# Kernel tuning notes

Hardware: AMD Instinct MI355X
Metric: run time of the kernel (lower is better)

Reference implementation:

```python
import jax, jax.numpy as jnp
import numpy as np
import math

CUTOFF = 5.0
F = 128
N_ATOMS = 4096
N_EDGES = 16384

# ---------- Clebsch-Gordan coefficients in the real spherical-harmonic basis ----------

def _cgc(l1, l2, l3, m1, m2, m3):
    if m1 + m2 != m3 or l3 < abs(l1 - l2) or l3 > l1 + l2:
        return 0.0
    f = math.factorial
    pre = math.sqrt((2 * l3 + 1) * f(l3 + l1 - l2) * f(l3 - l1 + l2) * f(l1 + l2 - l3) / f(l1 + l2 + l3 + 1))
    pre *= math.sqrt(f(l3 + m3) * f(l3 - m3) * f(l1 - m1) * f(l1 + m1) * f(l2 - m2) * f(l2 + m2))
    s = 0.0
    for k in range(l1 + l2 - l3 + 1):
        a = [k, l1 + l2 - l3 - k, l1 - m1 - k, l2 + m2 - k, l3 - l2 + m1 + k, l3 - l1 - m2 + k]
        if min(a) < 0:
            continue
        d = 1.0
        for t in a:
            d *= f(t)
        s += (-1) ** k / d
    return pre * s

def _umat(l):
    # complex SH in terms of real SH (rows: complex m, cols: real m, offset by l)
    U = np.zeros((2 * l + 1, 2 * l + 1), dtype=np.complex128)
    U[l, l] = 1.0
    for m in range(1, l + 1):
        U[l + m, l + m] = (-1) ** m / math.sqrt(2)
        U[l + m, l - m] = 1j * (-1) ** m / math.sqrt(2)
        U[l - m, l + m] = 1.0 / math.sqrt(2)
        U[l - m, l - m] = -1j / math.sqrt(2)
    return U

def _real_cg(l1, l2, l3):
    cg = np.zeros((2 * l1 + 1, 2 * l2 + 1, 2 * l3 + 1), dtype=np.complex128)
    for i, m1 in enumerate(range(-l1, l1 + 1)):
        for j, m2 in enumerate(range(-l2, l2 + 1)):
            m3 = m1 + m2
            if abs(m3) <= l3:
                cg[i, j, l3 + m3] = _cgc(l1, l2, l3, m1, m2, m3)
    U1, U2, U3 = _umat(l1), _umat(l2), _umat(l3)
    C = np.einsum('abc,aA,bB,cC->ABC', cg, U1, U2, np.conj(U3))
    return np.real(C).astype(np.float32)

# coupling paths (l1 from bond basis 0..2, l2 from atom features 0..4, output l3 0..4);
# even l1+l2+l3 keeps proper tensors only (include_pseudotensors=False)
PATHS = [(l1, l2, l3) for l1 in range(3) for l2 in range(5) for l3 in range(5)
         if abs(l1 - l2) <= l3 <= l1 + l2 and (l1 + l2 + l3) % 2 == 0]
CG_TABLES = [_real_cg(*p) for p in PATHS]

# ---------- equivariant building blocks ----------

def _seg(l):
    return slice(l * l, (l + 1) * (l + 1))

def edense(x, W, b):
    # per-degree channel mixing; bias only on the scalar (l=0) channel
    L = W.shape[0] - 1
    outs = []
    for l in range(L + 1):
        o = jnp.einsum('epmf,fg->epmg', x[:, :, _seg(l), :], W[l])
        if l == 0:
            o = o + b
        outs.append(o)
    return jnp.concatenate(outs, axis=-2)

def normalize(x, eps=1e-6):
    n2 = jnp.sum(x * x, axis=-2, keepdims=True)
    return x * jax.lax.rsqrt(n2 + eps)

def gated_mish(x):
    s = x[..., 0:1, :]
    sp = jax.nn.softplus(s)
    t = jnp.tanh(sp)
    ms = s * t
    dm = t + s * (1.0 - t * t) * jax.nn.sigmoid(s)
    return jnp.concatenate([ms, x[..., 1:, :] * dm], axis=-2)

def real_sph_harm(u):
    # Racah-normalized real SH up to l=2, m ordered -l..l (cartesian_order=False)
    x, y, z = u[:, 0], u[:, 1], u[:, 2]
    s3 = math.sqrt(3.0)
    return jnp.stack([
        jnp.ones_like(x),
        y, z, x,
        s3 * x * y, s3 * y * z, 0.5 * (3.0 * z * z - 1.0), s3 * x * z, 0.5 * s3 * (x * x - y * y),
    ], axis=-1)  # (E, 9)

def basis_expansion(disp):
    r = jnp.sqrt(jnp.sum(disp * disp, axis=-1) + 1e-12)  # (E,)
    sh = real_sph_harm(disp / r[:, None])                 # (E, 9)
    k = jnp.arange(F, dtype=disp.dtype)
    rad = jnp.cos(k[None, :] * (jnp.pi * r[:, None] / CUTOFF))  # basic_fourier, (E, F)
    uc = r / CUTOFF
    denom = jnp.maximum(1.0 - uc * uc, 1e-9)
    cut = jnp.where(uc < 1.0, jnp.exp(1.0 - 1.0 / denom), 0.0)  # smooth_cutoff
    rad = rad * cut[:, None]
    return sh[:, None, :, None] * rad[:, None, None, :]  # (E, 1, 9, F)

def tensor_product(x1, x2, w_tp):
    # CG tensor product (FusedTensor math): per-path learnable per-feature weights
    E, Ff = x1.shape[0], x1.shape[-1]
    out = jnp.zeros((E, 1, 25, Ff), dtype=x1.dtype)
    for p, (l1, l2, l3) in enumerate(PATHS):
        C = jnp.asarray(CG_TABLES[p])
        a = x1[:, 0, _seg(l1), :]
        b = x2[:, 0, _seg(l2), :]
        seg = jnp.einsum('abc,eaf,ebf->ecf', C, a, b)
        out = out.at[:, 0, _seg(l3), :].add(seg * w_tp[p][None, None, :])
    return out

# ---------- harness ----------

def setup_inputs() -> dict:
    key = jax.random.key(0)
    ks = jax.random.split(key, 8)
    sc = 1.0 / math.sqrt(F)
    return {
        'atomic_descriptors': jax.random.normal(ks[0], (N_ATOMS, 1, 25, F), jnp.float32),
        'neighbour_indices': jax.random.randint(ks[1], (N_EDGES, 2), 0, N_ATOMS),
        'neighbour_displacements': jax.random.normal(ks[2], (N_EDGES, 3), jnp.float32),
        'W1': jax.random.normal(ks[3], (5, F, F), jnp.float32) * sc,
        'b1': jnp.zeros((F,), jnp.float32),
        'W2': jax.random.normal(ks[4], (5, F, F), jnp.float32) * sc,
        'b2': jnp.zeros((F,), jnp.float32),
        'W3': jax.random.normal(ks[5], (3, F, F), jnp.float32) * sc,
        'b3': jnp.zeros((F,), jnp.float32),
        'w_tp': jax.random.normal(ks[6], (len(PATHS), F), jnp.float32),
    }

def reference(atomic_descriptors, neighbour_indices, neighbour_displacements, W1, b1, W2, b2, W3, b3, w_tp):
    i, j = neighbour_indices[:, 0], neighbour_indices[:, 1]
    y = atomic_descriptors[i] + atomic_descriptors[j]       # (E, 1, 25, F)
    y = edense(y, W1, b1)
    y = normalize(y)
    y = gated_mish(y)
    y = edense(y, W2, b2) + y
    be = basis_expansion(neighbour_displacements)           # (E, 1, 9, F)
    bd = edense(be, W3, b3)
    return tensor_product(bd, y, w_tp)                      # (E, 1, 25, F)
```

## Files before the change

### kernel.cpp

```cpp
#include <hip/hip_runtime.h>
#include <math.h>

#ifndef M_PI
#define M_PI 3.14159265358979323846
#endif

namespace {

constexpr int NF = 128;
constexpr int NM = 25;

struct CD { double re, im; };
constexpr CD cmulc(CD x, CD y){ return CD{x.re*y.re - x.im*y.im, x.re*y.im + x.im*y.re}; }

constexpr double cfact(int n){ double r = 1.0; for (int i = 2; i <= n; ++i) r *= (double)i; return r; }

constexpr double csqrt_(double x){
  if (x <= 0.0) return 0.0;
  double g = x < 1.0 ? 1.0 : x;
  for (int i = 0; i < 48; ++i) g = 0.5 * (g + x / g);
  return g;
}

constexpr double cgc_(int l1, int l2, int l3, int m1, int m2, int m3){
  if (m1 + m2 != m3) return 0.0;
  int dmin = l1 > l2 ? l1 - l2 : l2 - l1;
  if (l3 < dmin || l3 > l1 + l2) return 0.0;
  double pre = csqrt_((2.0*l3 + 1.0) * cfact(l3 + l1 - l2) * cfact(l3 - l1 + l2) *
                      cfact(l1 + l2 - l3) / cfact(l1 + l2 + l3 + 1));
  pre *= csqrt_(cfact(l3 + m3) * cfact(l3 - m3) * cfact(l1 - m1) * cfact(l1 + m1) *
                cfact(l2 - m2) * cfact(l2 + m2));
  double s = 0.0;
  for (int k = 0; k <= l1 + l2 - l3; ++k){
    int a0 = k, a1 = l1 + l2 - l3 - k, a2 = l1 - m1 - k;
    int a3 = l2 + m2 - k, a4 = l3 - l2 + m1 + k, a5 = l3 - l1 - m2 + k;
    if (a0 < 0 || a1 < 0 || a2 < 0 || a3 < 0 || a4 < 0 || a5 < 0) continue;
    double d = cfact(a0)*cfact(a1)*cfact(a2)*cfact(a3)*cfact(a4)*cfact(a5);
    s += ((k & 1) ? -1.0 : 1.0) / d;
  }
  return pre * s;
}

constexpr CD umat(int l, int a, int A){
  const double is2 = 0.70710678118654752440;
  int ma = a - l, mA = A - l;
  if (ma == 0) return (mA == 0) ? CD{1.0, 0.0} : CD{0.0, 0.0};
  if (ma > 0){
    double sg = (ma & 1) ? -1.0 : 1.0;
    if (mA ==  ma) return CD{sg * is2, 0.0};
    if (mA == -ma) return CD{0.0, sg * is2};
    return CD{0.0, 0.0};
  }
  if (mA == -ma) return CD{is2, 0.0};
  if (mA ==  ma) return CD{0.0, -is2};
  return CD{0.0, 0.0};
}

struct TpEntry { int a, b, c, p; float v; };
struct TpTable { TpEntry e[1024]; int n; int npaths; };

constexpr TpTable build_tp(){
  TpTable T{};
  T.n = 0;
  int p = 0;
  for (int l1 = 0; l1 < 3; ++l1)
  for (int l2 = 0; l2 < 5; ++l2)
  for (int l3 = 0; l3 < 5; ++l3){
    int dmin = l1 > l2 ? l1 - l2 : l2 - l1;
    if (l3 < dmin || l3 > l1 + l2) continue;
    if ((l1 + l2 + l3) & 1) continue;
    double Cr[5][9][9] = {};
    for (int a = 0; a <= 2*l1; ++a)
    for (int b = 0; b <= 2*l2; ++b){
      int m1 = a - l1, m2 = b - l2, m3 = m1 + m2;
      if (m3 < -l3 || m3 > l3) continue;
      double cg = cgc_(l1, l2, l3, m1, m2, m3);
      if (cg == 0.0) continue;
      int c3 = l3 + m3;
      int Al[2] = { l1 + m1, l1 - m1 }; int nA = (m1 == 0) ? 1 : 2;
      int Bl[2] = { l2 + m2, l2 - m2 }; int nB = (m2 == 0) ? 1 : 2;
      int Cl[2] = { l3 + m3, l3 - m3 }; int nC = (m3 == 0) ? 1 : 2;
      for (int ia = 0; ia < nA; ++ia)
      for (int ib = 0; ib < nB; ++ib)
      for (int ic = 0; ic < nC; ++ic){
        CD u1 = umat(l1, a, Al[ia]);
        CD u2 = umat(l2, b, Bl[ib]);
        CD u3 = umat(l3, c3, Cl[ic]);
        CD t12 = cmulc(u1, u2);
        double re = t12.re * u3.re + t12.im * u3.im;
        Cr[Al[ia]][Bl[ib]][Cl[ic]] += cg * re;
      }
    }
    for (int A = 0; A <= 2*l1; ++A)
    for (int B = 0; B <= 2*l2; ++B)
    for (int Cc = 0; Cc <= 2*l3; ++Cc){
      double v = Cr[A][B][Cc];
      if (v > 1e-12 || v < -1e-12){
        T.e[T.n].a = l1*l1 + A;
        T.e[T.n].b = l2*l2 + B;
        T.e[T.n].c = l3*l3 + Cc;
        T.e[T.n].p = p;
        T.e[T.n].v = (float)v;
        ++T.n;
      }
    }
    ++p;
  }
  T.npaths = p;
  return T;
}

constexpr TpTable TPT = build_tp();
constexpr int TPN      = TPT.n;
constexpr int NPATHS_C = TPT.npaths;
static_assert(NPATHS_C == 23, "path count mismatch vs reference PATHS");
static_assert(TPN <= 1024, "TP table overflow");

struct TpSorted { TpEntry e[1024]; int n; int split; };
constexpr TpSorted sort_tp(){
  TpSorted S{}; S.n = TPT.n; S.split = 0;
  int k = 0;
  for (int half = 0; half < 2; ++half){
    for (int b = 0; b < NM; ++b)
      for (int t = 0; t < TPT.n; ++t){
        int h = (TPT.e[t].c >= 13) ? 1 : 0;
        if (h == half && TPT.e[t].b == b) S.e[k++] = TPT.e[t];
      }
    if (half == 0) S.split = k;
  }
  return S;
}
constexpr TpSorted STP = sort_tp();
static_assert(STP.n == TPN, "sort lost entries");
constexpr int TP_SPLIT = STP.split;

using bfrag = __attribute__((ext_vector_type(8))) short;
using f32x4 = __attribute__((ext_vector_type(4))) float;

__device__ __forceinline__ unsigned short bf16rn(float x){
  unsigned u = __float_as_uint(x);
  unsigned r = (u + 0x7FFFu + ((u >> 16) & 1u)) >> 16;
  return (unsigned short)r;
}
__device__ __forceinline__ float bfhi_to_f(unsigned short h){
  return __uint_as_float((unsigned)h << 16);
}

constexpr int T_STRIDE = 136;
constexpr int Y_STRIDE = 129;

__global__ __launch_bounds__(256) void prep_kernel(const float* __restrict__ W1,
                                                   const float* __restrict__ W2,
                                                   const float* __restrict__ W3,
                                                   short* __restrict__ W1hi, short* __restrict__ W1lo,
                                                   short* __restrict__ W2hi, short* __restrict__ W2lo,
                                                   short* __restrict__ W3hi, short* __restrict__ W3lo){
  const int t = blockIdx.x * 256 + threadIdx.x;
  if (t >= 26624) return;
  int arr, s;
  if (t < 10240)      { arr = 0; s = t; }
  else if (t < 20480) { arr = 1; s = t - 10240; }
  else                { arr = 2; s = t - 20480; }
  const int lane = s & 63;
  const int ks   = (s >> 6) & 3;
  const int nt   = (s >> 8) & 7;
  const int l    = s >> 11;
  const float* W = (arr == 0) ? W1 : (arr == 1) ? W2 : W3;
  short* Hi = (arr == 0) ? W1hi : (arr == 1) ? W2hi : W3hi;
  short* Lo = (arr == 0) ? W1lo : (arr == 1) ? W2lo : W3lo;
  const int g = 16 * nt + (lane & 15);
  short hi8[8], lo8[8];
  #pragma unroll
  for (int j = 0; j < 8; ++j){
    const int f = 32 * ks + 8 * (lane >> 4) + j;
    const float w = W[(l * NF + f) * NF + g];
    unsigned short h = bf16rn(w);
    hi8[j] = (short)h;
    lo8[j] = (short)bf16rn(w - bfhi_to_f(h));
  }
  const size_t off = (size_t)s * 8;
  *(bfrag*)(Hi + off) = *(bfrag*)hi8;
  *(bfrag*)(Lo + off) = *(bfrag*)lo8;
}

__device__ __forceinline__ void mfma_gemm(const unsigned short* tHi, const unsigned short* tLo,
                                          const short* __restrict__ Whi, const short* __restrict__ Wlo,
                                          int lane, int wave, f32x4 acc[5][2]){
  const int quad = lane >> 4, l16 = lane & 15;
  #pragma unroll
  for (int l = 0; l < 5; ++l){
    const int mb = l * l;
    #pragma unroll
    for (int ks = 0; ks < 4; ++ks){
      const bfrag ah = *(const bfrag*)&tHi[(mb + l16) * T_STRIDE + 32 * ks + 8 * quad];
      const bfrag al = *(const bfrag*)&tLo[(mb + l16) * T_STRIDE + 32 * ks + 8 * quad];
      #pragma unroll
      for (int n2 = 0; n2 < 2; ++n2){
        const int nt = 2 * wave + n2;
        const size_t off = ((size_t)((l * 8 + nt) * 4 + ks)) * 512 + lane * 8;
        const bfrag bh = *(const bfrag*)(Whi + off);
        const bfrag bl = *(const bfrag*)(Wlo + off);
        acc[l][n2] = __builtin_amdgcn_mfma_f32_16x16x32_bf16(ah, bh, acc[l][n2], 0, 0, 0);
        acc[l][n2] = __builtin_amdgcn_mfma_f32_16x16x32_bf16(al, bh, acc[l][n2], 0, 0, 0);
        acc[l][n2] = __builtin_amdgcn_mfma_f32_16x16x32_bf16(ah, bl, acc[l][n2], 0, 0, 0);
      }
    }
  }
}

__global__ __launch_bounds__(256, 4) void atoms_kernel(const float* __restrict__ A,
                                                       const short* __restrict__ W1hi,
                                                       const short* __restrict__ W1lo,
                                                       float* __restrict__ Z){
  __shared__ unsigned short aHi[32 * T_STRIDE];
  __shared__ unsigned short aLo[32 * T_STRIDE];
  const int n   = blockIdx.x;
  const int tid = threadIdx.x;
  const int f   = tid & 127, half = tid >> 7;
  const float* Ab = A + (size_t)n * NM * NF;

  const int m0 = half ? 13 : 0, m1 = half ? 25 : 13;
  for (int m = m0; m < m1; ++m){
    const float x = Ab[m * NF + f];
    const unsigned short h = bf16rn(x);
    aHi[m * T_STRIDE + f] = h;
    aLo[m * T_STRIDE + f] = bf16rn(x - bfhi_to_f(h));
  }
  if (half){
    for (int m = 25; m < 32; ++m){ aHi[m * T_STRIDE + f] = 0; aLo[m * T_STRIDE + f] = 0; }
  }
  __syncthreads();

  const int lane = tid & 63, wave = tid >> 6;
  f32x4 acc[5][2];
  #pragma unroll
  for (int l = 0; l < 5; ++l)
    #pragma unroll
    for (int n2 = 0; n2 < 2; ++n2)
      acc[l][n2] = f32x4{0.f, 0.f, 0.f, 0.f};

  mfma_gemm(aHi, aLo, W1hi, W1lo, lane, wave, acc);

  const int quad = lane >> 4, l16 = lane & 15;
  float* Zb = Z + (size_t)n * NM * NF;
  #pragma unroll
  for (int l = 0; l < 5; ++l)
    #pragma unroll
    for (int n2 = 0; n2 < 2; ++n2){
      const int col = 16 * (2 * wave + n2) + l16;
      #pragma unroll
      for (int r = 0; r < 4; ++r){
        if (r <= 2 * l){
          const int row = 4 * quad + r;
          if (row <= 2 * l)
            Zb[(l * l + row) * NF + col] = acc[l][n2][r];
        }
      }
    }
}

__global__ __launch_bounds__(256) void radial_kernel(const float* __restrict__ disp,
                                                     const short* __restrict__ W3hi,
                                                     const short* __restrict__ W3lo,
                                                     const float* __restrict__ b3,
                                                     float* __restrict__ out,
                                                     int n_edges){
  __shared__ unsigned short rHi[32 * T_STRIDE];
  __shared__ unsigned short rLo[32 * T_STRIDE];
  __shared__ float rbuf[32];
  __shared__ float cbuf[32];
  const int e0  = blockIdx.x * 32;
  const int tid = threadIdx.x;
  if (tid < 32){
    const int e = e0 + tid;
    float r = 1.f, cut = 0.f;
    if (e < n_edges){
      const float dx = disp[3 * e], dy = disp[3 * e + 1], dz = disp[3 * e + 2];
      r = sqrtf(dx * dx + dy * dy + dz * dz + 1e-12f);
      const float uc  = r * 0.2f;
      const float den = fmaxf(1.f - uc * uc, 1e-9f);
      cut = (uc < 1.f) ? expf(1.f - 1.f / den) : 0.f;
    }
    rbuf[tid] = r; cbuf[tid] = cut;
  }
  __syncthreads();

  const int f = tid & 127, half = tid >> 7;
  #pragma unroll
  for (int mr = 0; mr < 16; ++mr){
    const int m = half * 16 + mr;
    const float rad = cosf((float)f * ((float)M_PI * 0.2f) * rbuf[m]) * cbuf[m];
    const unsigned short h = bf16rn(rad);
    rHi[m * T_STRIDE + f] = h;
    rLo[m * T_STRIDE + f] = bf16rn(rad - bfhi_to_f(h));
  }
  __syncthreads();

  const int lane = tid & 63, wave = tid >> 6, quad = lane >> 4, l16 = lane & 15;
  f32x4 acc[2][3][2];
  #pragma unroll
  for (int mt = 0; mt < 2; ++mt)
    #pragma unroll
    for (int l = 0; l < 3; ++l)
      #pragma unroll
      for (int n2 = 0; n2 < 2; ++n2)
        acc[mt][l][n2] = f32x4{0.f, 0.f, 0.f, 0.f};

  #pragma unroll
  for (int mt = 0; mt < 2; ++mt){
    #pragma unroll
    for (int ks = 0; ks < 4; ++ks){
      const bfrag ah = *(const bfrag*)&rHi[(mt * 16 + l16) * T_STRIDE + 32 * ks + 8 * quad];
      const bfrag al = *(const bfrag*)&rLo[(mt * 16 + l16) * T_STRIDE + 32 * ks + 8 * quad];
      #pragma unroll
      for (int l = 0; l < 3; ++l){
        #pragma unroll
        for (int n2 = 0; n2 < 2; ++n2){
          const int nt = 2 * wave + n2;
          const size_t off = ((size_t)((l * 8 + nt) * 4 + ks)) * 512 + lane * 8;
          const bfrag bh = *(const bfrag*)(W3hi + off);
          const bfrag bl = *(const bfrag*)(W3lo + off);
          acc[mt][l][n2] = __builtin_amdgcn_mfma_f32_16x16x32_bf16(ah, bh, acc[mt][l][n2], 0, 0, 0);
          acc[mt][l][n2] = __builtin_amdgcn_mfma_f32_16x16x32_bf16(al, bh, acc[mt][l][n2], 0, 0, 0);
          acc[mt][l][n2] = __builtin_amdgcn_mfma_f32_16x16x32_bf16(ah, bl, acc[mt][l][n2], 0, 0, 0);
        }
      }
    }
  }

  #pragma unroll
  for (int mt = 0; mt < 2; ++mt)
    #pragma unroll
    for (int l = 0; l < 3; ++l)
      #pragma unroll
      for (int n2 = 0; n2 < 2; ++n2){
        const int col = 16 * (2 * wave + n2) + l16;
        #pragma unroll
        for (int rr = 0; rr < 4; ++rr){
          const int e = e0 + mt * 16 + 4 * quad + rr;
          if (e < n_edges){
            float v = acc[mt][l][n2][rr];
            if (l == 0) v += b3[col];
            out[(size_t)e * (NM * NF) + l * NF + col] = v;
          }
        }
      }
}

template<int CG>
__device__ __forceinline__ void tp_accum(const float* y2col ,
                                         const float bd[9], const float wp[NPATHS_C],
                                         float o[13]){
  constexpr int t0 = (CG == 0) ? 0 : TP_SPLIT;
  constexpr int t1 = (CG == 0) ? TP_SPLIT : TPN;
  constexpr int cbase = (CG == 0) ? 0 : 13;
  float y2b = 0.f;
  #pragma unroll
  for (int t = t0; t < t1; ++t){
    if (t == t0 || STP.e[t].b != STP.e[t-1].b)
      y2b = y2col[STP.e[t].b * Y_STRIDE];
    o[STP.e[t].c - cbase] = fmaf(STP.e[t].v * wp[STP.e[t].p],
                                 bd[STP.e[t].a] * y2b,
                                 o[STP.e[t].c - cbase]);
  }
}

__global__ __launch_bounds__(256, 5) void edge_kernel(const float* __restrict__ Z,
                                                      const int*   __restrict__ nbr,
                                                      const float* __restrict__ disp,
                                                      const float* __restrict__ b1,
                                                      const short* __restrict__ W2hi,
                                                      const short* __restrict__ W2lo,
                                                      const float* __restrict__ b2,
                                                      const float* __restrict__ wtp,
                                                      float* __restrict__ out){
  __shared__ unsigned short tHi[32 * T_STRIDE];
  __shared__ unsigned short tLo[32 * T_STRIDE];
  __shared__ float y2_lds[NM * Y_STRIDE];
  __shared__ float nbuf[2 * NF];
  __shared__ float y0buf[NF];

  const int e   = blockIdx.x;
  const int tid = threadIdx.x;
  const int f   = tid & 127, half = tid >> 7;
  const int i = nbr[2 * e], j = nbr[2 * e + 1];
  const float* Zi = Z + (size_t)i * NM * NF;
  const float* Zj = Z + (size_t)j * NM * NF;

  const float dx = disp[3 * e], dy = disp[3 * e + 1], dz = disp[3 * e + 2];
  const float r  = sqrtf(dx * dx + dy * dy + dz * dz + 1e-12f);

  float vreg[13];
  float n2 = 0.f;
  if (!half){
    #pragma unroll
    for (int k = 0; k < 13; ++k){
      float v = Zi[k * NF + f] + Zj[k * NF + f];
      if (k == 0) v += b1[f];
      vreg[k] = v;
      n2 = fmaf(v, v, n2);
    }
    y0buf[f] = vreg[0];
  } else {
    #pragma unroll
    for (int k = 0; k < 12; ++k){
      const float v = Zi[(13 + k) * NF + f] + Zj[(13 + k) * NF + f];
      vreg[k] = v;
      n2 = fmaf(v, v, n2);
    }
  }
  nbuf[half * NF + f] = n2;
  __syncthreads();

  const float inv = 1.0f / sqrtf(nbuf[f] + nbuf[NF + f] + 1e-6f);
  const float s   = y0buf[f] * inv;
  const float sp  = fmaxf(s, 0.f) + log1pf(expf(-fabsf(s)));
  const float th  = tanhf(sp);
  const float sg  = 1.0f / (1.0f + expf(-s));
  const float dm  = th + s * (1.f - th * th) * sg;
  if (!half){
    #pragma unroll
    for (int k = 0; k < 13; ++k){
      const float tv = (k == 0) ? (s * th) : (vreg[k] * inv * dm);
      const unsigned short h = bf16rn(tv);
      tHi[k * T_STRIDE + f] = h;
      tLo[k * T_STRIDE + f] = bf16rn(tv - bfhi_to_f(h));
    }
  } else {
    #pragma unroll
    for (int k = 0; k < 12; ++k){
      const float tv = vreg[k] * inv * dm;
      const unsigned short h = bf16rn(tv);
      tHi[(13 + k) * T_STRIDE + f] = h;
      tLo[(13 + k) * T_STRIDE + f] = bf16rn(tv - bfhi_to_f(h));
    }
    #pragma unroll
    for (int m = 25; m < 32; ++m){ tHi[m * T_STRIDE + f] = 0; tLo[m * T_STRIDE + f] = 0; }
  }
  __syncthreads();

  const int lane = tid & 63, wave = tid >> 6;
  f32x4 acc[5][2];
  #pragma unroll
  for (int l = 0; l < 5; ++l)
    #pragma unroll
    for (int c = 0; c < 2; ++c)
      acc[l][c] = f32x4{0.f, 0.f, 0.f, 0.f};

  mfma_gemm(tHi, tLo, W2hi, W2lo, lane, wave, acc);

  const int quad = lane >> 4, l16 = lane & 15;
  #pragma unroll
  for (int l = 0; l < 5; ++l)
    #pragma unroll
    for (int c = 0; c < 2; ++c){
      const int col = 16 * (2 * wave + c) + l16;
      #pragma unroll
      for (int rr = 0; rr < 4; ++rr){
        if (rr <= 2 * l){
          const int row = 4 * quad + rr;
          if (row <= 2 * l){
            const int m = l * l + row;
            float v = acc[l][c][rr]
                    + bfhi_to_f(tHi[m * T_STRIDE + col])
                    + bfhi_to_f(tLo[m * T_STRIDE + col]);
            if (l == 0) v += b2[col];
            y2_lds[m * Y_STRIDE + col] = v;
          }
        }
      }
    }
  __syncthreads();

  const float rinv = 1.0f / r;
  const float ux = dx * rinv, uy = dy * rinv, uz = dz * rinv;
  const float s3 = 1.7320508075688772f;
  const size_t ebase = (size_t)e * (NM * NF);
  float bd[9];
  {
    const float rw0 = out[ebase + f];
    const float rw1 = out[ebase + NF + f];
    const float rw2 = out[ebase + 2 * NF + f];
    bd[0] = rw0;
    bd[1] = uy * rw1;
    bd[2] = uz * rw1;
    bd[3] = ux * rw1;
    bd[4] = (s3 * ux * uy) * rw2;
    bd[5] = (s3 * uy * uz) * rw2;
    bd[6] = (0.5f * (3.f * uz * uz - 1.f)) * rw2;
    bd[7] = (s3 * ux * uz) * rw2;
    bd[8] = (0.5f * s3 * (ux * ux - uy * uy)) * rw2;
  }
  float wp[NPATHS_C];
  #pragma unroll
  for (int p = 0; p < NPATHS_C; ++p) wp[p] = wtp[p * NF + f];

  float o[13];
  #pragma unroll
  for (int k = 0; k < 13; ++k) o[k] = 0.f;

  float* ob = out + ebase;
  if (!half){
    tp_accum<0>(&y2_lds[f], bd, wp, o);
    #pragma unroll
    for (int k = 0; k < 13; ++k) ob[k * NF + f] = o[k];
  } else {
    tp_accum<1>(&y2_lds[f], bd, wp, o);
    #pragma unroll
    for (int k = 0; k < 12; ++k) ob[(13 + k) * NF + f] = o[k];
  }
}

}

extern "C" void kernel_launch(void* const* d_in, const int* in_sizes, int n_in,
                              void* d_out, int out_size, void* d_ws, size_t ws_size,
                              hipStream_t stream) {
  (void)n_in; (void)out_size;
  const float* A    = (const float*)d_in[0];
  const int*   nbr  = (const int*)  d_in[1];
  const float* disp = (const float*)d_in[2];
  const float* W1   = (const float*)d_in[3];
  const float* b1   = (const float*)d_in[4];
  const float* W2   = (const float*)d_in[5];
  const float* b2   = (const float*)d_in[6];
  const float* W3   = (const float*)d_in[7];
  const float* b3   = (const float*)d_in[8];
  const float* wtp  = (const float*)d_in[9];
  float* out = (float*)d_out;

  const int n_atoms = in_sizes[0] / (NM * NF);
  const int n_edges = in_sizes[1] / 2;

  const size_t wsz   = (size_t)5 * 8 * 4 * 64 * 8 * sizeof(short);
  const size_t wsz3  = (size_t)3 * 8 * 4 * 64 * 8 * sizeof(short);
  const size_t w3off = 4 * wsz;
  const size_t zoff  = w3off + 2 * wsz3;
  const size_t need  = zoff + (size_t)n_atoms * NM * NF * sizeof(float);
  if (ws_size < need) return;

  short* W1hi = (short*)((char*)d_ws + 0 * wsz);
  short* W1lo = (short*)((char*)d_ws + 1 * wsz);
  short* W2hi = (short*)((char*)d_ws + 2 * wsz);
  short* W2lo = (short*)((char*)d_ws + 3 * wsz);
  short* W3hi = (short*)((char*)d_ws + w3off);
  short* W3lo = (short*)((char*)d_ws + w3off + wsz3);
  float* Z    = (float*)((char*)d_ws + zoff);

  prep_kernel<<<dim3(104), dim3(256), 0, stream>>>(W1, W2, W3, W1hi, W1lo,
                                                   W2hi, W2lo, W3hi, W3lo);
  atoms_kernel<<<dim3(n_atoms), dim3(256), 0, stream>>>(A, W1hi, W1lo, Z);
  radial_kernel<<<dim3((n_edges + 31) / 32), dim3(256), 0, stream>>>(disp, W3hi, W3lo,
                                                                     b3, out, n_edges);
  edge_kernel<<<dim3(n_edges), dim3(256), 0, stream>>>(Z, nbr, disp, b1, W2hi, W2lo,
                                                       b2, wtp, out);
}
```

Baseline: 585.6 us.

## Process two items per block to reuse weight fragments, merge atom and radial kernels

Each 512-thread block now handles two atoms or two edges, with each wave owning one 16-column N tile. Every B-fragment of the bf16 hi/lo weights is loaded once and applied to both items' A fragments, which halves global weight traffic per item. The atom GEMM and the radial GEMM are merged into one launch, split by block index, which saves a kernel launch and lets the two stages overlap. The larger blocks use more LDS and registers per block and add an extra barrier in the edge kernel, which may lower occupancy.

```diff
diff --git a/kernel.cpp b/kernel.cpp
--- a/kernel.cpp
+++ b/kernel.cpp
@@ -183,172 +183,173 @@
   *(bfrag*)(Lo + off) = *(bfrag*)lo8;
 }
 
-__device__ __forceinline__ void mfma_gemm(const unsigned short* tHi, const unsigned short* tLo,
-                                          const short* __restrict__ Whi, const short* __restrict__ Wlo,
-                                          int lane, int wave, f32x4 acc[5][2]){
+__device__ __forceinline__ void mfma_gemm2(const unsigned short* tHi0, const unsigned short* tLo0,
+                                           const unsigned short* tHi1, const unsigned short* tLo1,
+                                           const short* __restrict__ Whi, const short* __restrict__ Wlo,
+                                           int lane, int wave, f32x4 acc[5][2]){
   const int quad = lane >> 4, l16 = lane & 15;
   #pragma unroll
   for (int l = 0; l < 5; ++l){
     const int mb = l * l;
     #pragma unroll
     for (int ks = 0; ks < 4; ++ks){
-      const bfrag ah = *(const bfrag*)&tHi[(mb + l16) * T_STRIDE + 32 * ks + 8 * quad];
-      const bfrag al = *(const bfrag*)&tLo[(mb + l16) * T_STRIDE + 32 * ks + 8 * quad];
-      #pragma unroll
-      for (int n2 = 0; n2 < 2; ++n2){
-        const int nt = 2 * wave + n2;
-        const size_t off = ((size_t)((l * 8 + nt) * 4 + ks)) * 512 + lane * 8;
-        const bfrag bh = *(const bfrag*)(Whi + off);
-        const bfrag bl = *(const bfrag*)(Wlo + off);
-        acc[l][n2] = __builtin_amdgcn_mfma_f32_16x16x32_bf16(ah, bh, acc[l][n2], 0, 0, 0);
-        acc[l][n2] = __builtin_amdgcn_mfma_f32_16x16x32_bf16(al, bh, acc[l][n2], 0, 0, 0);
-        acc[l][n2] = __builtin_amdgcn_mfma_f32_16x16x32_bf16(ah, bl, acc[l][n2], 0, 0, 0);
-      }
-    }
-  }
-}
-
-__global__ __launch_bounds__(256, 4) void atoms_kernel(const float* __restrict__ A,
-                                                       const short* __restrict__ W1hi,
-                                                       const short* __restrict__ W1lo,
-                                                       float* __restrict__ Z){
-  __shared__ unsigned short aHi[32 * T_STRIDE];
-  __shared__ unsigned short aLo[32 * T_STRIDE];
-  const int n   = blockIdx.x;
-  const int tid = threadIdx.x;
-  const int f   = tid & 127, half = tid >> 7;
-  const float* Ab = A + (size_t)n * NM * NF;
-
-  const int m0 = half ? 13 : 0, m1 = half ? 25 : 13;
-  for (int m = m0; m < m1; ++m){
-    const float x = Ab[m * NF + f];
-    const unsigned short h = bf16rn(x);
-    aHi[m * T_STRIDE + f] = h;
-    aLo[m * T_STRIDE + f] = bf16rn(x - bfhi_to_f(h));
-  }
-  if (half){
-    for (int m = 25; m < 32; ++m){ aHi[m * T_STRIDE + f] = 0; aLo[m * T_STRIDE + f] = 0; }
-  }
-  __syncthreads();
-
-  const int lane = tid & 63, wave = tid >> 6;
-  f32x4 acc[5][2];
-  #pragma unroll
-  for (int l = 0; l < 5; ++l)
-    #pragma unroll
-    for (int n2 = 0; n2 < 2; ++n2)
-      acc[l][n2] = f32x4{0.f, 0.f, 0.f, 0.f};
-
-  mfma_gemm(aHi, aLo, W1hi, W1lo, lane, wave, acc);
-
-  const int quad = lane >> 4, l16 = lane & 15;
-  float* Zb = Z + (size_t)n * NM * NF;
-  #pragma unroll
-  for (int l = 0; l < 5; ++l)
-    #pragma unroll
-    for (int n2 = 0; n2 < 2; ++n2){
-      const int col = 16 * (2 * wave + n2) + l16;
-      #pragma unroll
-      for (int r = 0; r < 4; ++r){
-        if (r <= 2 * l){
-          const int row = 4 * quad + r;
-          if (row <= 2 * l)
-            Zb[(l * l + row) * NF + col] = acc[l][n2][r];
-        }
-      }
-    }
-}
-
-__global__ __launch_bounds__(256) void radial_kernel(const float* __restrict__ disp,
+      const size_t off = ((size_t)((l * 8 + wave) * 4 + ks)) * 512 + lane * 8;
+      const bfrag bh = *(const bfrag*)(Whi + off);
+      const bfrag bl = *(const bfrag*)(Wlo + off);
+      const int aoff = (mb + l16) * T_STRIDE + 32 * ks + 8 * quad;
+      {
+        const bfrag ah = *(const bfrag*)&tHi0[aoff];
+        const bfrag al = *(const bfrag*)&tLo0[aoff];
+        acc[l][0] = __builtin_amdgcn_mfma_f32_16x16x32_bf16(ah, bh, acc[l][0], 0, 0, 0);
+        acc[l][0] = __builtin_amdgcn_mfma_f32_16x16x32_bf16(al, bh, acc[l][0], 0, 0, 0);
+        acc[l][0] = __builtin_amdgcn_mfma_f32_16x16x32_bf16(ah, bl, acc[l][0], 0, 0, 0);
+      }
+      {
+        const bfrag ah = *(const bfrag*)&tHi1[aoff];
+        const bfrag al = *(const bfrag*)&tLo1[aoff];
+        acc[l][1] = __builtin_amdgcn_mfma_f32_16x16x32_bf16(ah, bh, acc[l][1], 0, 0, 0);
+        acc[l][1] = __builtin_amdgcn_mfma_f32_16x16x32_bf16(al, bh, acc[l][1], 0, 0, 0);
+        acc[l][1] = __builtin_amdgcn_mfma_f32_16x16x32_bf16(ah, bl, acc[l][1], 0, 0, 0);
+      }
+    }
+  }
+}
+
+__global__ __launch_bounds__(512, 4) void mid_kernel(const float* __restrict__ A,
+                                                     const short* __restrict__ W1hi,
+                                                     const short* __restrict__ W1lo,
+                                                     float* __restrict__ Z,
+                                                     const float* __restrict__ disp,
                                                      const short* __restrict__ W3hi,
                                                      const short* __restrict__ W3lo,
                                                      const float* __restrict__ b3,
                                                      float* __restrict__ out,
-                                                     int n_edges){
-  __shared__ unsigned short rHi[32 * T_STRIDE];
-  __shared__ unsigned short rLo[32 * T_STRIDE];
-  __shared__ float rbuf[32];
-  __shared__ float cbuf[32];
-  const int e0  = blockIdx.x * 32;
-  const int tid = threadIdx.x;
-  if (tid < 32){
-    const int e = e0 + tid;
-    float r = 1.f, cut = 0.f;
-    if (e < n_edges){
-      const float dx = disp[3 * e], dy = disp[3 * e + 1], dz = disp[3 * e + 2];
-      r = sqrtf(dx * dx + dy * dy + dz * dz + 1e-12f);
-      const float uc  = r * 0.2f;
-      const float den = fmaxf(1.f - uc * uc, 1e-9f);
-      cut = (uc < 1.f) ? expf(1.f - 1.f / den) : 0.f;
-    }
-    rbuf[tid] = r; cbuf[tid] = cut;
-  }
-  __syncthreads();
-
-  const int f = tid & 127, half = tid >> 7;
-  #pragma unroll
-  for (int mr = 0; mr < 16; ++mr){
-    const int m = half * 16 + mr;
-    const float rad = cosf((float)f * ((float)M_PI * 0.2f) * rbuf[m]) * cbuf[m];
-    const unsigned short h = bf16rn(rad);
-    rHi[m * T_STRIDE + f] = h;
-    rLo[m * T_STRIDE + f] = bf16rn(rad - bfhi_to_f(h));
-  }
-  __syncthreads();
-
-  const int lane = tid & 63, wave = tid >> 6, quad = lane >> 4, l16 = lane & 15;
-  f32x4 acc[2][3][2];
-  #pragma unroll
-  for (int mt = 0; mt < 2; ++mt)
-    #pragma unroll
-    for (int l = 0; l < 3; ++l)
+                                                     int n_atoms, int n_edges, int nA2){
+  __shared__ unsigned short sHi[2][32 * T_STRIDE];
+  __shared__ unsigned short sLo[2][32 * T_STRIDE];
+  __shared__ float rbuf[64];
+  __shared__ float cbuf[64];
+
+  const int tid  = threadIdx.x;
+  const int f    = tid & 127;
+  const int q    = tid >> 7;
+  const int lane = tid & 63, wave = tid >> 6;
+  const int quad = lane >> 4, l16 = lane & 15;
+
+  if ((int)blockIdx.x < nA2){
+    const int as   = q >> 1;
+    const int half = q & 1;
+    int a = 2 * blockIdx.x + as;
+    if (a >= n_atoms) a = n_atoms - 1;
+    const float* Ab = A + (size_t)a * NM * NF;
+    unsigned short* hi = sHi[as];
+    unsigned short* lo = sLo[as];
+    const int m0 = half ? 13 : 0, m1 = half ? 25 : 13;
+    for (int m = m0; m < m1; ++m){
+      const float x = Ab[m * NF + f];
+      const unsigned short h = bf16rn(x);
+      hi[m * T_STRIDE + f] = h;
+      lo[m * T_STRIDE + f] = bf16rn(x - bfhi_to_f(h));
+    }
+    if (half){
+      for (int m = 25; m < 32; ++m){ hi[m * T_STRIDE + f] = 0; lo[m * T_STRIDE + f] = 0; }
+    }
+    __syncthreads();
+
+    f32x4 acc[5][2];
+    #pragma unroll
+    for (int l = 0; l < 5; ++l){ acc[l][0] = f32x4{0,0,0,0}; acc[l][1] = f32x4{0,0,0,0}; }
+    mfma_gemm2(sHi[0], sLo[0], sHi[1], sLo[1], W1hi, W1lo, lane, wave, acc);
+
+    #pragma unroll
+    for (int as2 = 0; as2 < 2; ++as2){
+      int aa = 2 * blockIdx.x + as2;
+      if (aa >= n_atoms) aa = n_atoms - 1;
+      float* Zb = Z + (size_t)aa * NM * NF;
+      const int col = 16 * wave + l16;
       #pragma unroll
-      for (int n2 = 0; n2 < 2; ++n2)
-        acc[mt][l][n2] = f32x4{0.f, 0.f, 0.f, 0.f};
-
-  #pragma unroll
-  for (int mt = 0; mt < 2; ++mt){
-    #pragma unroll
-    for (int ks = 0; ks < 4; ++ks){
-      const bfrag ah = *(const bfrag*)&rHi[(mt * 16 + l16) * T_STRIDE + 32 * ks + 8 * quad];
-      const bfrag al = *(const bfrag*)&rLo[(mt * 16 + l16) * T_STRIDE + 32 * ks + 8 * quad];
+      for (int l = 0; l < 5; ++l)
+        #pragma unroll
+        for (int r = 0; r < 4; ++r){
+          if (r <= 2 * l){
+            const int row = 4 * quad + r;
+            if (row <= 2 * l)
+              Zb[(l * l + row) * NF + col] = acc[l][as2][r];
+          }
+        }
+    }
+  } else {
+    const int e0 = (blockIdx.x - nA2) * 64;
+    if (tid < 64){
+      const int e = e0 + tid;
+      float r = 1.f, cut = 0.f;
+      if (e < n_edges){
+        const float dx = disp[3 * e], dy = disp[3 * e + 1], dz = disp[3 * e + 2];
+        r = sqrtf(dx * dx + dy * dy + dz * dz + 1e-12f);
+        const float uc  = r * 0.2f;
+        const float den = fmaxf(1.f - uc * uc, 1e-9f);
+        cut = (uc < 1.f) ? expf(1.f - 1.f / den) : 0.f;
+      }
+      rbuf[tid] = r; cbuf[tid] = cut;
+    }
+    __syncthreads();
+
+    unsigned short* hi = &sHi[0][0];
+    unsigned short* lo = &sLo[0][0];
+    #pragma unroll
+    for (int mr = 0; mr < 16; ++mr){
+      const int m = q * 16 + mr;
+      const float rad = cosf((float)f * ((float)M_PI * 0.2f) * rbuf[m]) * cbuf[m];
+      const unsigned short h = bf16rn(rad);
+      hi[m * T_STRIDE + f] = h;
+      lo[m * T_STRIDE + f] = bf16rn(rad - bfhi_to_f(h));
+    }
+    __syncthreads();
+
+    f32x4 acc[4][3];
+    #pragma unroll
+    for (int mt = 0; mt < 4; ++mt)
       #pragma unroll
-      for (int l = 0; l < 3; ++l){
+      for (int l = 0; l < 3; ++l) acc[mt][l] = f32x4{0,0,0,0};
+
+    #pragma unroll
+    for (int l = 0; l < 3; ++l){
+      #pragma unroll
+      for (int ks = 0; ks < 4; ++ks){
+        const size_t off = ((size_t)((l * 8 + wave) * 4 + ks)) * 512 + lane * 8;
+        const bfrag bh = *(const bfrag*)(W3hi + off);
+        const bfrag bl = *(const bfrag*)(W3lo + off);
         #pragma unroll
-        for (int n2 = 0; n2 < 2; ++n2){
-          const int nt = 2 * wave + n2;
-          const size_t off = ((size_t)((l * 8 + nt) * 4 + ks)) * 512 + lane * 8;
-          const bfrag bh = *(const bfrag*)(W3hi + off);
-          const bfrag bl = *(const bfrag*)(W3lo + off);
-          acc[mt][l][n2] = __builtin_amdgcn_mfma_f32_16x16x32_bf16(ah, bh, acc[mt][l][n2], 0, 0, 0);
-          acc[mt][l][n2] = __builtin_amdgcn_mfma_f32_16x16x32_bf16(al, bh, acc[mt][l][n2], 0, 0, 0);
-          acc[mt][l][n2] = __builtin_amdgcn_mfma_f32_16x16x32_bf16(ah, bl, acc[mt][l][n2], 0, 0, 0);
+        for (int mt = 0; mt < 4; ++mt){
+          const int aoff = (mt * 16 + l16) * T_STRIDE + 32 * ks + 8 * quad;
+          const bfrag ah = *(const bfrag*)&hi[aoff];
+          const bfrag al = *(const bfrag*)&lo[aoff];
+          acc[mt][l] = __builtin_amdgcn_mfma_f32_16x16x32_bf16(ah, bh, acc[mt][l], 0, 0, 0);
+          acc[mt][l] = __builtin_amdgcn_mfma_f32_16x16x32_bf16(al, bh, acc[mt][l], 0, 0, 0);
+          acc[mt][l] = __builtin_amdgcn_mfma_f32_16x16x32_bf16(ah, bl, acc[mt][l], 0, 0, 0);
         }
       }
     }
-  }
-
-  #pragma unroll
-  for (int mt = 0; mt < 2; ++mt)
-    #pragma unroll
-    for (int l = 0; l < 3; ++l)
+
+    const int col = 16 * wave + l16;
+    #pragma unroll
+    for (int mt = 0; mt < 4; ++mt)
       #pragma unroll
-      for (int n2 = 0; n2 < 2; ++n2){
-        const int col = 16 * (2 * wave + n2) + l16;
+      for (int l = 0; l < 3; ++l)
         #pragma unroll
         for (int rr = 0; rr < 4; ++rr){
           const int e = e0 + mt * 16 + 4 * quad + rr;
           if (e < n_edges){
-            float v = acc[mt][l][n2][rr];
+            float v = acc[mt][l][rr];
             if (l == 0) v += b3[col];
             out[(size_t)e * (NM * NF) + l * NF + col] = v;
           }
         }
-      }
+  }
 }
 
 template<int CG>
-__device__ __forceinline__ void tp_accum(const float* y2col ,
+__device__ __forceinline__ void tp_accum(const float* y2col,
                                          const float bd[9], const float wp[NPATHS_C],
                                          float o[13]){
   constexpr int t0 = (CG == 0) ? 0 : TP_SPLIT;
@@ -365,7 +366,7 @@
   }
 }
 
-__global__ __launch_bounds__(256, 5) void edge_kernel(const float* __restrict__ Z,
+__global__ __launch_bounds__(512, 4) void edge_kernel(const float* __restrict__ Z,
                                                       const int*   __restrict__ nbr,
                                                       const float* __restrict__ disp,
                                                       const float* __restrict__ b1,
@@ -373,16 +374,22 @@
                                                       const short* __restrict__ W2lo,
                                                       const float* __restrict__ b2,
                                                       const float* __restrict__ wtp,
-                                                      float* __restrict__ out){
-  __shared__ unsigned short tHi[32 * T_STRIDE];
-  __shared__ unsigned short tLo[32 * T_STRIDE];
-  __shared__ float y2_lds[NM * Y_STRIDE];
-  __shared__ float nbuf[2 * NF];
-  __shared__ float y0buf[NF];
-
-  const int e   = blockIdx.x;
-  const int tid = threadIdx.x;
-  const int f   = tid & 127, half = tid >> 7;
+                                                      float* __restrict__ out,
+                                                      int n_edges){
+  __shared__ unsigned short tHi[2][32 * T_STRIDE];
+  __shared__ unsigned short tLo[2][32 * T_STRIDE];
+  __shared__ float y2_lds[2][NM * Y_STRIDE];
+  __shared__ float nbuf[4 * NF];
+  __shared__ float y0buf[2][NF];
+
+  const int tid  = threadIdx.x;
+  const int f    = tid & 127;
+  const int q    = tid >> 7;
+  const int es   = q >> 1;
+  const int half = q & 1;
+
+  int e = 2 * blockIdx.x + es;
+  if (e >= n_edges) e = n_edges - 1;
   const int i = nbr[2 * e], j = nbr[2 * e + 1];
   const float* Zi = Z + (size_t)i * NM * NF;
   const float* Zj = Z + (size_t)j * NM * NF;
@@ -400,7 +407,7 @@
       vreg[k] = v;
       n2 = fmaf(v, v, n2);
     }
-    y0buf[f] = vreg[0];
+    y0buf[es][f] = vreg[0];
   } else {
     #pragma unroll
     for (int k = 0; k < 12; ++k){
@@ -409,67 +416,66 @@
       n2 = fmaf(v, v, n2);
     }
   }
-  nbuf[half * NF + f] = n2;
+  nbuf[(es * 2 + half) * NF + f] = n2;
   __syncthreads();
 
-  const float inv = 1.0f / sqrtf(nbuf[f] + nbuf[NF + f] + 1e-6f);
-  const float s   = y0buf[f] * inv;
+  const float inv = 1.0f / sqrtf(nbuf[(es * 2) * NF + f] + nbuf[(es * 2 + 1) * NF + f] + 1e-6f);
+  const float s   = y0buf[es][f] * inv;
   const float sp  = fmaxf(s, 0.f) + log1pf(expf(-fabsf(s)));
   const float th  = tanhf(sp);
   const float sg  = 1.0f / (1.0f + expf(-s));
   const float dm  = th + s * (1.f - th * th) * sg;
+  unsigned short* hi = tHi[es];
+  unsigned short* lo = tLo[es];
   if (!half){
     #pragma unroll
     for (int k = 0; k < 13; ++k){
       const float tv = (k == 0) ? (s * th) : (vreg[k] * inv * dm);
       const unsigned short h = bf16rn(tv);
-      tHi[k * T_STRIDE + f] = h;
-      tLo[k * T_STRIDE + f] = bf16rn(tv - bfhi_to_f(h));
+      hi[k * T_STRIDE + f] = h;
+      lo[k * T_STRIDE + f] = bf16rn(tv - bfhi_to_f(h));
     }
   } else {
     #pragma unroll
     for (int k = 0; k < 12; ++k){
       const float tv = vreg[k] * inv * dm;
       const unsigned short h = bf16rn(tv);
-      tHi[(13 + k) * T_STRIDE + f] = h;
-      tLo[(13 + k) * T_STRIDE + f] = bf16rn(tv - bfhi_to_f(h));
-    }
-    #pragma unroll
-    for (int m = 25; m < 32; ++m){ tHi[m * T_STRIDE + f] = 0; tLo[m * T_STRIDE + f] = 0; }
+      hi[(13 + k) * T_STRIDE + f] = h;
+      lo[(13 + k) * T_STRIDE + f] = bf16rn(tv - bfhi_to_f(h));
+    }
+    #pragma unroll
+    for (int m = 25; m < 32; ++m){ hi[m * T_STRIDE + f] = 0; lo[m * T_STRIDE + f] = 0; }
   }
   __syncthreads();
 
   const int lane = tid & 63, wave = tid >> 6;
   f32x4 acc[5][2];
   #pragma unroll
-  for (int l = 0; l < 5; ++l)
-    #pragma unroll
-    for (int c = 0; c < 2; ++c)
-      acc[l][c] = f32x4{0.f, 0.f, 0.f, 0.f};
-
-  mfma_gemm(tHi, tLo, W2hi, W2lo, lane, wave, acc);
+  for (int l = 0; l < 5; ++l){ acc[l][0] = f32x4{0,0,0,0}; acc[l][1] = f32x4{0,0,0,0}; }
+
+  mfma_gemm2(tHi[0], tLo[0], tHi[1], tLo[1], W2hi, W2lo, lane, wave, acc);
 
   const int quad = lane >> 4, l16 = lane & 15;
-  #pragma unroll
-  for (int l = 0; l < 5; ++l)
-    #pragma unroll
-    for (int c = 0; c < 2; ++c){
-      const int col = 16 * (2 * wave + c) + l16;
+  const int col = 16 * wave + l16;
+  #pragma unroll
+  for (int es2 = 0; es2 < 2; ++es2){
+    #pragma unroll
+    for (int l = 0; l < 5; ++l)
       #pragma unroll
       for (int rr = 0; rr < 4; ++rr){
         if (rr <= 2 * l){
           const int row = 4 * quad + rr;
           if (row <= 2 * l){
             const int m = l * l + row;
-            float v = acc[l][c][rr]
-                    + bfhi_to_f(tHi[m * T_STRIDE + col])
-                    + bfhi_to_f(tLo[m * T_STRIDE + col]);
+            float v = acc[l][es2][rr]
+                    + bfhi_to_f(tHi[es2][m * T_STRIDE + col])
+                    + bfhi_to_f(tLo[es2][m * T_STRIDE + col]);
             if (l == 0) v += b2[col];
-            y2_lds[m * Y_STRIDE + col] = v;
+            y2_lds[es2][m * Y_STRIDE + col] = v;
           }
         }
       }
-    }
+  }
   __syncthreads();
 
   const float rinv = 1.0f / r;
@@ -494,6 +500,7 @@
   float wp[NPATHS_C];
   #pragma unroll
   for (int p = 0; p < NPATHS_C; ++p) wp[p] = wtp[p * NF + f];
+  __syncthreads();
 
   float o[13];
   #pragma unroll
@@ -501,11 +508,11 @@
 
   float* ob = out + ebase;
   if (!half){
-    tp_accum<0>(&y2_lds[f], bd, wp, o);
+    tp_accum<0>(&y2_lds[es][f], bd, wp, o);
     #pragma unroll
     for (int k = 0; k < 13; ++k) ob[k * NF + f] = o[k];
   } else {
-    tp_accum<1>(&y2_lds[f], bd, wp, o);
+    tp_accum<1>(&y2_lds[es][f], bd, wp, o);
     #pragma unroll
     for (int k = 0; k < 12; ++k) ob[(13 + k) * NF + f] = o[k];
   }
@@ -547,11 +554,15 @@
   short* W3lo = (short*)((char*)d_ws + w3off + wsz3);
   float* Z    = (float*)((char*)d_ws + zoff);
 
+  const int nA2 = (n_atoms + 1) / 2;
+  const int nR  = (n_edges + 63) / 64;
+
   prep_kernel<<<dim3(104), dim3(256), 0, stream>>>(W1, W2, W3, W1hi, W1lo,
                                                    W2hi, W2lo, W3hi, W3lo);
-  atoms_kernel<<<dim3(n_atoms), dim3(256), 0, stream>>>(A, W1hi, W1lo, Z);
-  radial_kernel<<<dim3((n_edges + 31) / 32), dim3(256), 0, stream>>>(disp, W3hi, W3lo,
-                                                                     b3, out, n_edges);
-  edge_kernel<<<dim3(n_edges), dim3(256), 0, stream>>>(Z, nbr, disp, b1, W2hi, W2lo,
-                                                       b2, wtp, out);
-}
+  mid_kernel<<<dim3(nA2 + nR), dim3(512), 0, stream>>>(A, W1hi, W1lo, Z, disp,
+                                                       W3hi, W3lo, b3, out,
+                                                       n_atoms, n_edges, nA2);
+  edge_kernel<<<dim3((n_edges + 1) / 2), dim3(512), 0, stream>>>(Z, nbr, disp, b1,
+                                                                 W2hi, W2lo, b2, wtp,
+                                                                 out, n_edges);
+}
```

Result: faster. 539.9 us (-7.8%).
